# Kernel tuning notes

Hardware: AMD Instinct MI355X
Metric: run time of the kernel (lower is better)

The kernel has to match this reference:

```python
import jax, jax.numpy as jnp
import numpy as np

B, P, E, D = 256, 2048, 16, 2
HID, OUT = 128, 128
BN_EPS = 1e-5


def setup_inputs() -> dict:
    key = jax.random.key(0)
    ks = jax.random.split(key, 16)
    inp = {
        "barcode_h0": jax.random.normal(ks[0], (B, P, D), jnp.float32),
        "barcode_h0_count": jax.random.randint(ks[1], (B,), 0, P),
        "barcode_h1": jax.random.normal(ks[2], (B, P, D), jnp.float32),
        "barcode_h1_count": jax.random.randint(ks[3], (B,), 0, P),
        # SLayer params (one per homology dim): centers ~ U[0,1), log_sharpness = log(3.0)
        "centers0": jax.random.uniform(ks[4], (E, D), jnp.float32),
        "log_sharp0": jnp.full((E, D), np.log(3.0), jnp.float32),
        "centers1": jax.random.uniform(ks[5], (E, D), jnp.float32),
        "log_sharp1": jnp.full((E, D), np.log(3.0), jnp.float32),
        # head: Linear(2E -> HID, no bias), BN, ReLU, Linear(HID -> OUT, no bias), BN
        "W1": jax.random.normal(ks[6], (2 * E, HID), jnp.float32) / np.sqrt(2 * E),
        "gamma1": jnp.ones((HID,), jnp.float32),
        "beta1": jnp.zeros((HID,), jnp.float32),
        "W2": jax.random.normal(ks[7], (HID, OUT), jnp.float32) / np.sqrt(HID),
        "gamma2": jnp.ones((OUT,), jnp.float32),
        "beta2": jnp.zeros((OUT,), jnp.float32),
    }
    return inp


def _slayer(pts, counts, centers, log_sharp):
    # pts: [B,P,2], counts: [B], centers/log_sharp: [E,2]
    sharp = jax.nn.softplus(log_sharp) + 1e-6                       # [E,2]
    diff = pts[:, :, None, :] - centers[None, None, :, :]           # [B,P,E,2]
    resp = jnp.exp(-jnp.sum(sharp * diff * diff, axis=-1))          # [B,P,E]
    mask = (jnp.arange(pts.shape[1])[None, :] < counts[:, None]).astype(resp.dtype)
    return jnp.sum(resp * mask[:, :, None], axis=1)                 # [B,E]


def _batchnorm_train(x, gamma, beta):
    m = jnp.mean(x, axis=0)
    v = jnp.var(x, axis=0)  # biased, as torch uses for normalization
    return (x - m) * jax.lax.rsqrt(v + BN_EPS) * gamma + beta


def reference(barcode_h0, barcode_h0_count, barcode_h1, barcode_h1_count,
              centers0, log_sharp0, centers1, log_sharp1,
              W1, gamma1, beta1, W2, gamma2, beta2):
    f0 = _slayer(barcode_h0, barcode_h0_count, centers0, log_sharp0)  # [B,E]
    f1 = _slayer(barcode_h1, barcode_h1_count, centers1, log_sharp1)  # [B,E]
    x = jnp.concatenate([f0, f1], axis=1)                             # [B,2E]
    h = jax.nn.relu(_batchnorm_train(x @ W1, gamma1, beta1))          # [B,HID]
    y = _batchnorm_train(h @ W2, gamma2, beta2)                       # [B,OUT]
    norm = jnp.maximum(jnp.linalg.norm(y, axis=1, keepdims=True), 1e-12)
    return y / norm
```

## Files before the change

kernel.cpp:

```cpp
#include <hip/hip_runtime.h>

#define Bsz 256
#define Pn  2048
#define En  16
#define HIDn 128
#define OUTn 128
#define BN_EPS 1e-5f

__global__ __launch_bounds__(256) void k_slayer_w1(
    const float* __restrict__ pts0, const int* __restrict__ cnt0,
    const float* __restrict__ pts1, const int* __restrict__ cnt1,
    const float* __restrict__ c0, const float* __restrict__ ls0,
    const float* __restrict__ c1, const float* __restrict__ ls1,
    const float* __restrict__ W1,
    float* __restrict__ u)
{
    __shared__ float cen[2][En][2];
    __shared__ float shp[2][En][2];
    __shared__ float red[4][32];
    __shared__ float xrow[32];

    const int tid = threadIdx.x;
    const int b   = blockIdx.x;

    if (tid < 64) {
        int h = tid >> 5, r = tid & 31, e = r >> 1, d = r & 1;
        const float* C = h ? c1 : c0;
        const float* L = h ? ls1 : ls0;
        cen[h][e][d] = C[e * 2 + d];
        float z  = L[e * 2 + d];
        float sp = (z > 20.f) ? z : logf(1.f + expf(z));
        shp[h][e][d] = sp + 1e-6f;
    }
    __syncthreads();

    float acc0[En], acc1[En];
    #pragma unroll
    for (int e = 0; e < En; e++) { acc0[e] = 0.f; acc1[e] = 0.f; }

    const int n0 = cnt0[b];
    const int n1 = cnt1[b];
    const float2* p0 = (const float2*)pts0 + (size_t)b * Pn;
    const float2* p1 = (const float2*)pts1 + (size_t)b * Pn;

    for (int p = tid; p < n0; p += 256) {
        float2 pt = p0[p];
        #pragma unroll
        for (int e = 0; e < En; e++) {
            float dx = pt.x - cen[0][e][0];
            float dy = pt.y - cen[0][e][1];
            float t  = shp[0][e][0] * dx * dx + shp[0][e][1] * dy * dy;
            acc0[e] += __expf(-t);
        }
    }
    for (int p = tid; p < n1; p += 256) {
        float2 pt = p1[p];
        #pragma unroll
        for (int e = 0; e < En; e++) {
            float dx = pt.x - cen[1][e][0];
            float dy = pt.y - cen[1][e][1];
            float t  = shp[1][e][0] * dx * dx + shp[1][e][1] * dy * dy;
            acc1[e] += __expf(-t);
        }
    }

    #pragma unroll
    for (int e = 0; e < En; e++) {
        #pragma unroll
        for (int off = 32; off > 0; off >>= 1) {
            acc0[e] += __shfl_down(acc0[e], off, 64);
            acc1[e] += __shfl_down(acc1[e], off, 64);
        }
    }
    const int wave = tid >> 6, lane = tid & 63;
    if (lane == 0) {
        #pragma unroll
        for (int e = 0; e < En; e++) { red[wave][e] = acc0[e]; red[wave][16 + e] = acc1[e]; }
    }
    __syncthreads();
    if (tid < 32) xrow[tid] = red[0][tid] + red[1][tid] + red[2][tid] + red[3][tid];
    __syncthreads();

    if (tid < HIDn) {
        float a = 0.f;
        #pragma unroll
        for (int k = 0; k < 32; k++) a = fmaf(xrow[k], W1[k * HIDn + tid], a);
        u[b * HIDn + tid] = a;
    }
}

__global__ __launch_bounds__(128) void k_bn1_w2(
    const float* __restrict__ u, const float* __restrict__ W2,
    const float* __restrict__ g1, const float* __restrict__ be1,
    float* __restrict__ ypre)
{
    __shared__ float hrow[HIDn];
    const int j = threadIdx.x, b = blockIdx.x;

    float s = 0.f, sq = 0.f, uv = 0.f;
    #pragma unroll 8
    for (int bb = 0; bb < Bsz; bb++) {
        float v = u[bb * HIDn + j];
        s += v; sq = fmaf(v, v, sq);
        if (bb == b) uv = v;
    }
    float m    = s * (1.f / Bsz);
    float var  = sq * (1.f / Bsz) - m * m;
    float rstd = rsqrtf(var + BN_EPS);
    float h    = fmaxf((uv - m) * rstd * g1[j] + be1[j], 0.f);
    hrow[j] = h;
    __syncthreads();

    float a = 0.f;
    #pragma unroll 8
    for (int k = 0; k < HIDn; k++) a = fmaf(hrow[k], W2[k * OUTn + j], a);
    ypre[b * OUTn + j] = a;
}

__global__ __launch_bounds__(128) void k_bn2_norm(
    const float* __restrict__ ypre,
    const float* __restrict__ g2, const float* __restrict__ be2,
    float* __restrict__ out)
{
    __shared__ float part[2];
    const int j = threadIdx.x, b = blockIdx.x;

    float s = 0.f, sq = 0.f, yv = 0.f;
    #pragma unroll 8
    for (int bb = 0; bb < Bsz; bb++) {
        float v = ypre[bb * OUTn + j];
        s += v; sq = fmaf(v, v, sq);
        if (bb == b) yv = v;
    }
    float m    = s * (1.f / Bsz);
    float var  = sq * (1.f / Bsz) - m * m;
    float rstd = rsqrtf(var + BN_EPS);
    float y    = (yv - m) * rstd * g2[j] + be2[j];

    float s2 = y * y;
    #pragma unroll
    for (int off = 32; off > 0; off >>= 1) s2 += __shfl_down(s2, off, 64);
    if ((j & 63) == 0) part[j >> 6] = s2;
    __syncthreads();
    float total = part[0] + part[1];
    float norm  = fmaxf(sqrtf(total), 1e-12f);
    out[b * OUTn + j] = y / norm;
}

extern "C" void kernel_launch(void* const* d_in, const int* in_sizes, int n_in,
                              void* d_out, int out_size, void* d_ws, size_t ws_size,
                              hipStream_t stream) {
    const float* pts0 = (const float*)d_in[0];
    const int*   cnt0 = (const int*)  d_in[1];
    const float* pts1 = (const float*)d_in[2];
    const int*   cnt1 = (const int*)  d_in[3];
    const float* c0   = (const float*)d_in[4];
    const float* ls0  = (const float*)d_in[5];
    const float* c1   = (const float*)d_in[6];
    const float* ls1  = (const float*)d_in[7];
    const float* W1   = (const float*)d_in[8];
    const float* g1   = (const float*)d_in[9];
    const float* be1  = (const float*)d_in[10];
    const float* W2   = (const float*)d_in[11];
    const float* g2   = (const float*)d_in[12];
    const float* be2  = (const float*)d_in[13];
    float* out = (float*)d_out;

    float* ws   = (float*)d_ws;
    float* u    = ws;
    float* ypre = ws + 32768;

    k_slayer_w1<<<Bsz, 256, 0, stream>>>(pts0, cnt0, pts1, cnt1,
                                         c0, ls0, c1, ls1, W1, u);
    k_bn1_w2<<<Bsz, 128, 0, stream>>>(u, W2, g1, be1, ypre);
    k_bn2_norm<<<Bsz, 128, 0, stream>>>(ypre, g2, be2, out);
}
```

Before: 120.1 us.

## Fuse SLayer, head and batch norms into one cooperative grid-synced kernel

Replaces the three launches with a single cooperative kernel of 512-thread blocks that uses grid.sync between stages. Batch-norm statistics are now computed once per feature column and published through the workspace, instead of every block rescanning the full activation matrix. The SLayer loop is also changed: the quadratic is expanded into precomputed exp2 coefficients, and all points are processed branch-free, with masked points pushed far away so their response is zero. The cost is four grid-wide barriers and a reliance on all 256 blocks being co-resident.

Result: slower. 231.6 us (+92.8%).

```diff
diff --git a/kernel.cpp b/kernel.cpp
--- a/kernel.cpp
+++ b/kernel.cpp
@@ -1,177 +1,226 @@
 #include <hip/hip_runtime.h>
-
-#define Bsz 256
-#define Pn  2048
-#define En  16
+#include <hip/hip_cooperative_groups.h>
+
+namespace cg = cooperative_groups;
+
+#define Bsz  256
+#define Pn   2048
+#define En   16
 #define HIDn 128
 #define OUTn 128
 #define BN_EPS 1e-5f
 
-__global__ __launch_bounds__(256) void k_slayer_w1(
-    const float* __restrict__ pts0, const int* __restrict__ cnt0,
-    const float* __restrict__ pts1, const int* __restrict__ cnt1,
-    const float* __restrict__ c0, const float* __restrict__ ls0,
-    const float* __restrict__ c1, const float* __restrict__ ls1,
-    const float* __restrict__ W1,
-    float* __restrict__ u)
+struct Params {
+    const float *pts0, *pts1;
+    const int   *cnt0, *cnt1;
+    const float *c0, *ls0, *c1, *ls1;
+    const float *W1, *g1, *be1, *W2, *g2, *be2;
+    float *out;
+    float *u, *ypre, *m1, *r1, *m2, *r2;
+};
+
+__global__ __launch_bounds__(512) void fused(Params P)
 {
-    __shared__ float cen[2][En][2];
-    __shared__ float shp[2][En][2];
-    __shared__ float red[4][32];
-    __shared__ float xrow[32];
+    cg::grid_group grid = cg::this_grid();
+
+    __shared__ float cst[2][En][5];
+    __shared__ float red[8][32];
+    __shared__ float row[128];
 
     const int tid = threadIdx.x;
     const int b   = blockIdx.x;
 
-    if (tid < 64) {
-        int h = tid >> 5, r = tid & 31, e = r >> 1, d = r & 1;
-        const float* C = h ? c1 : c0;
-        const float* L = h ? ls1 : ls0;
-        cen[h][e][d] = C[e * 2 + d];
-        float z  = L[e * 2 + d];
-        float sp = (z > 20.f) ? z : logf(1.f + expf(z));
-        shp[h][e][d] = sp + 1e-6f;
-    }
-    __syncthreads();
-
-    float acc0[En], acc1[En];
+    if (tid < 32) {
+        int h = tid >> 4, e = tid & 15;
+        const float* C = h ? P.c1 : P.c0;
+        const float* L = h ? P.ls1 : P.ls0;
+        float cx = C[e * 2 + 0], cy = C[e * 2 + 1];
+        float z0 = L[e * 2 + 0], z1 = L[e * 2 + 1];
+        float s0 = ((z0 > 20.f) ? z0 : logf(1.f + expf(z0))) + 1e-6f;
+        float s1 = ((z1 > 20.f) ? z1 : logf(1.f + expf(z1))) + 1e-6f;
+        const float L2E = 1.44269504088896340736f;
+        float q0 = s0 * L2E, q1 = s1 * L2E;
+        cst[h][e][0] = -q0;
+        cst[h][e][1] = 2.f * q0 * cx;
+        cst[h][e][2] = -q1;
+        cst[h][e][3] = 2.f * q1 * cy;
+        cst[h][e][4] = -(q0 * cx * cx + q1 * cy * cy);
+    }
+    __syncthreads();
+
+    float acc[32];
     #pragma unroll
-    for (int e = 0; e < En; e++) { acc0[e] = 0.f; acc1[e] = 0.f; }
-
-    const int n0 = cnt0[b];
-    const int n1 = cnt1[b];
-    const float2* p0 = (const float2*)pts0 + (size_t)b * Pn;
-    const float2* p1 = (const float2*)pts1 + (size_t)b * Pn;
-
-    for (int p = tid; p < n0; p += 256) {
-        float2 pt = p0[p];
+    for (int i = 0; i < 32; i++) acc[i] = 0.f;
+
+    const int n0 = P.cnt0[b];
+    const int n1 = P.cnt1[b];
+    const float2* p0 = (const float2*)P.pts0 + (size_t)b * Pn;
+    const float2* p1 = (const float2*)P.pts1 + (size_t)b * Pn;
+
+    #pragma unroll
+    for (int k = 0; k < 4; k++) {
+        const int p = tid + k * 512;
+        float2 a = p0[p];
+        float2 c = p1[p];
+        float ax = (p < n0) ? a.x : 1e18f;
+        float ay = (p < n0) ? a.y : 0.f;
+        float cx = (p < n1) ? c.x : 1e18f;
+        float cy = (p < n1) ? c.y : 0.f;
+        float ax2 = ax * ax, ay2 = ay * ay;
+        float cx2 = cx * cx, cy2 = cy * cy;
         #pragma unroll
         for (int e = 0; e < En; e++) {
-            float dx = pt.x - cen[0][e][0];
-            float dy = pt.y - cen[0][e][1];
-            float t  = shp[0][e][0] * dx * dx + shp[0][e][1] * dy * dy;
-            acc0[e] += __expf(-t);
-        }
-    }
-    for (int p = tid; p < n1; p += 256) {
-        float2 pt = p1[p];
-        #pragma unroll
-        for (int e = 0; e < En; e++) {
-            float dx = pt.x - cen[1][e][0];
-            float dy = pt.y - cen[1][e][1];
-            float t  = shp[1][e][0] * dx * dx + shp[1][e][1] * dy * dy;
-            acc1[e] += __expf(-t);
+            float t = cst[0][e][4];
+            t = fmaf(cst[0][e][0], ax2, t);
+            t = fmaf(cst[0][e][1], ax,  t);
+            t = fmaf(cst[0][e][2], ay2, t);
+            t = fmaf(cst[0][e][3], ay,  t);
+            acc[e] += exp2f(t);
+            float s = cst[1][e][4];
+            s = fmaf(cst[1][e][0], cx2, s);
+            s = fmaf(cst[1][e][1], cx,  s);
+            s = fmaf(cst[1][e][2], cy2, s);
+            s = fmaf(cst[1][e][3], cy,  s);
+            acc[16 + e] += exp2f(s);
         }
     }
 
     #pragma unroll
-    for (int e = 0; e < En; e++) {
-        #pragma unroll
-        for (int off = 32; off > 0; off >>= 1) {
-            acc0[e] += __shfl_down(acc0[e], off, 64);
-            acc1[e] += __shfl_down(acc1[e], off, 64);
-        }
+    for (int i = 0; i < 32; i++) {
+        float v = acc[i];
+        #pragma unroll
+        for (int off = 32; off > 0; off >>= 1) v += __shfl_down(v, off, 64);
+        acc[i] = v;
     }
     const int wave = tid >> 6, lane = tid & 63;
     if (lane == 0) {
         #pragma unroll
-        for (int e = 0; e < En; e++) { red[wave][e] = acc0[e]; red[wave][16 + e] = acc1[e]; }
-    }
-    __syncthreads();
-    if (tid < 32) xrow[tid] = red[0][tid] + red[1][tid] + red[2][tid] + red[3][tid];
-    __syncthreads();
-
+        for (int i = 0; i < 32; i++) red[wave][i] = acc[i];
+    }
+    __syncthreads();
+    if (tid < 32) {
+        float s = 0.f;
+        #pragma unroll
+        for (int w = 0; w < 8; w++) s += red[w][tid];
+        row[tid] = s;
+    }
+    __syncthreads();
+
+    float u_reg = 0.f;
     if (tid < HIDn) {
-        float a = 0.f;
-        #pragma unroll
-        for (int k = 0; k < 32; k++) a = fmaf(xrow[k], W1[k * HIDn + tid], a);
-        u[b * HIDn + tid] = a;
-    }
-}
-
-__global__ __launch_bounds__(128) void k_bn1_w2(
-    const float* __restrict__ u, const float* __restrict__ W2,
-    const float* __restrict__ g1, const float* __restrict__ be1,
-    float* __restrict__ ypre)
-{
-    __shared__ float hrow[HIDn];
-    const int j = threadIdx.x, b = blockIdx.x;
-
-    float s = 0.f, sq = 0.f, uv = 0.f;
-    #pragma unroll 8
-    for (int bb = 0; bb < Bsz; bb++) {
-        float v = u[bb * HIDn + j];
-        s += v; sq = fmaf(v, v, sq);
-        if (bb == b) uv = v;
-    }
-    float m    = s * (1.f / Bsz);
-    float var  = sq * (1.f / Bsz) - m * m;
-    float rstd = rsqrtf(var + BN_EPS);
-    float h    = fmaxf((uv - m) * rstd * g1[j] + be1[j], 0.f);
-    hrow[j] = h;
-    __syncthreads();
-
-    float a = 0.f;
-    #pragma unroll 8
-    for (int k = 0; k < HIDn; k++) a = fmaf(hrow[k], W2[k * OUTn + j], a);
-    ypre[b * OUTn + j] = a;
-}
-
-__global__ __launch_bounds__(128) void k_bn2_norm(
-    const float* __restrict__ ypre,
-    const float* __restrict__ g2, const float* __restrict__ be2,
-    float* __restrict__ out)
-{
-    __shared__ float part[2];
-    const int j = threadIdx.x, b = blockIdx.x;
-
-    float s = 0.f, sq = 0.f, yv = 0.f;
-    #pragma unroll 8
-    for (int bb = 0; bb < Bsz; bb++) {
-        float v = ypre[bb * OUTn + j];
-        s += v; sq = fmaf(v, v, sq);
-        if (bb == b) yv = v;
-    }
-    float m    = s * (1.f / Bsz);
-    float var  = sq * (1.f / Bsz) - m * m;
-    float rstd = rsqrtf(var + BN_EPS);
-    float y    = (yv - m) * rstd * g2[j] + be2[j];
-
-    float s2 = y * y;
-    #pragma unroll
-    for (int off = 32; off > 0; off >>= 1) s2 += __shfl_down(s2, off, 64);
-    if ((j & 63) == 0) part[j >> 6] = s2;
-    __syncthreads();
-    float total = part[0] + part[1];
-    float norm  = fmaxf(sqrtf(total), 1e-12f);
-    out[b * OUTn + j] = y / norm;
+        #pragma unroll
+        for (int k = 0; k < 32; k++) u_reg = fmaf(row[k], P.W1[k * HIDn + tid], u_reg);
+        P.u[b * HIDn + tid] = u_reg;
+    }
+    grid.sync();
+
+    {
+        float s = 0.f, q = 0.f;
+        if (b < HIDn && tid < Bsz) {
+            float x = P.u[tid * HIDn + b];
+            s = x; q = x * x;
+        }
+        #pragma unroll
+        for (int off = 32; off > 0; off >>= 1) {
+            s += __shfl_down(s, off, 64);
+            q += __shfl_down(q, off, 64);
+        }
+        if (lane == 0) { red[wave][0] = s; red[wave][1] = q; }
+        __syncthreads();
+        if (b < HIDn && tid == 0) {
+            float S = red[0][0] + red[1][0] + red[2][0] + red[3][0];
+            float Q = red[0][1] + red[1][1] + red[2][1] + red[3][1];
+            float m = S * (1.f / Bsz);
+            float var = Q * (1.f / Bsz) - m * m;
+            P.m1[b] = m;
+            P.r1[b] = rsqrtf(var + BN_EPS);
+        }
+    }
+    grid.sync();
+
+    float yp_reg = 0.f;
+    if (tid < HIDn) {
+        float m = P.m1[tid], r = P.r1[tid];
+        float h = fmaxf(fmaf((u_reg - m) * r, P.g1[tid], P.be1[tid]), 0.f);
+        row[tid] = h;
+    }
+    __syncthreads();
+    if (tid < HIDn) {
+        #pragma unroll 8
+        for (int k = 0; k < HIDn; k++) yp_reg = fmaf(row[k], P.W2[k * OUTn + tid], yp_reg);
+        P.ypre[b * OUTn + tid] = yp_reg;
+    }
+    grid.sync();
+
+    {
+        float s = 0.f, q = 0.f;
+        if (b < OUTn && tid < Bsz) {
+            float x = P.ypre[tid * OUTn + b];
+            s = x; q = x * x;
+        }
+        #pragma unroll
+        for (int off = 32; off > 0; off >>= 1) {
+            s += __shfl_down(s, off, 64);
+            q += __shfl_down(q, off, 64);
+        }
+        if (lane == 0) { red[wave][0] = s; red[wave][1] = q; }
+        __syncthreads();
+        if (b < OUTn && tid == 0) {
+            float S = red[0][0] + red[1][0] + red[2][0] + red[3][0];
+            float Q = red[0][1] + red[1][1] + red[2][1] + red[3][1];
+            float m = S * (1.f / Bsz);
+            float var = Q * (1.f / Bsz) - m * m;
+            P.m2[b] = m;
+            P.r2[b] = rsqrtf(var + BN_EPS);
+        }
+    }
+    grid.sync();
+
+    float y = 0.f;
+    if (tid < OUTn) {
+        float m = P.m2[tid], r = P.r2[tid];
+        y = fmaf((yp_reg - m) * r, P.g2[tid], P.be2[tid]);
+        float sq = y * y;
+        #pragma unroll
+        for (int off = 32; off > 0; off >>= 1) sq += __shfl_down(sq, off, 64);
+        if (lane == 0) red[wave][0] = sq;
+    }
+    __syncthreads();
+    if (tid < OUTn) {
+        float total = red[0][0] + red[1][0];
+        float norm  = fmaxf(sqrtf(total), 1e-12f);
+        P.out[b * OUTn + tid] = y / norm;
+    }
 }
 
 extern "C" void kernel_launch(void* const* d_in, const int* in_sizes, int n_in,
                               void* d_out, int out_size, void* d_ws, size_t ws_size,
                               hipStream_t stream) {
-    const float* pts0 = (const float*)d_in[0];
-    const int*   cnt0 = (const int*)  d_in[1];
-    const float* pts1 = (const float*)d_in[2];
-    const int*   cnt1 = (const int*)  d_in[3];
-    const float* c0   = (const float*)d_in[4];
-    const float* ls0  = (const float*)d_in[5];
-    const float* c1   = (const float*)d_in[6];
-    const float* ls1  = (const float*)d_in[7];
-    const float* W1   = (const float*)d_in[8];
-    const float* g1   = (const float*)d_in[9];
-    const float* be1  = (const float*)d_in[10];
-    const float* W2   = (const float*)d_in[11];
-    const float* g2   = (const float*)d_in[12];
-    const float* be2  = (const float*)d_in[13];
-    float* out = (float*)d_out;
-
-    float* ws   = (float*)d_ws;
-    float* u    = ws;
-    float* ypre = ws + 32768;
-
-    k_slayer_w1<<<Bsz, 256, 0, stream>>>(pts0, cnt0, pts1, cnt1,
-                                         c0, ls0, c1, ls1, W1, u);
-    k_bn1_w2<<<Bsz, 128, 0, stream>>>(u, W2, g1, be1, ypre);
-    k_bn2_norm<<<Bsz, 128, 0, stream>>>(ypre, g2, be2, out);
+    Params P;
+    P.pts0 = (const float*)d_in[0];
+    P.cnt0 = (const int*)  d_in[1];
+    P.pts1 = (const float*)d_in[2];
+    P.cnt1 = (const int*)  d_in[3];
+    P.c0   = (const float*)d_in[4];
+    P.ls0  = (const float*)d_in[5];
+    P.c1   = (const float*)d_in[6];
+    P.ls1  = (const float*)d_in[7];
+    P.W1   = (const float*)d_in[8];
+    P.g1   = (const float*)d_in[9];
+    P.be1  = (const float*)d_in[10];
+    P.W2   = (const float*)d_in[11];
+    P.g2   = (const float*)d_in[12];
+    P.be2  = (const float*)d_in[13];
+    P.out  = (float*)d_out;
+
+    float* ws = (float*)d_ws;
+    P.u    = ws;
+    P.ypre = ws + 32768;
+    P.m1   = ws + 65536;
+    P.r1   = P.m1 + 128;
+    P.m2   = P.r1 + 128;
+    P.r2   = P.m2 + 128;
+
+    void* args[] = { (void*)&P };
+    hipLaunchCooperativeKernel((const void*)fused, dim3(Bsz), dim3(512), args, 0, stream);
 }
```
